# Kernel optimization log

Measured on AMD Instinct MI355X. Metric: run time of the kernel, lower is better.

Reference implementation:

```python
import jax, jax.numpy as jnp
import numpy as np
from jax.ops import segment_sum

N = 100000
E = 1600000
IN_DIM = 128
HID_DIM = 128
OUT_DIM = 64
BN_EPS = 1e-5


def setup_inputs() -> dict:
    key = jax.random.key(0)
    ks = jax.random.split(key, 8)
    h = jax.random.normal(ks[0], (N, IN_DIM), dtype=jnp.float32)
    src = jax.random.randint(ks[1], (E,), 0, N, dtype=jnp.int32)
    dst = jax.random.randint(ks[2], (E,), 0, N, dtype=jnp.int32)
    # GraphConv weights (glorot-ish scale)
    W1 = jax.random.normal(ks[3], (IN_DIM, HID_DIM), dtype=jnp.float32) / np.sqrt(IN_DIM)
    b1 = jnp.zeros((HID_DIM,), dtype=jnp.float32)
    W2 = jax.random.normal(ks[4], (HID_DIM, OUT_DIM), dtype=jnp.float32) / np.sqrt(HID_DIM)
    b2 = jnp.zeros((OUT_DIM,), dtype=jnp.float32)
    gamma = jnp.ones((HID_DIM,), dtype=jnp.float32)
    beta = jnp.zeros((HID_DIM,), dtype=jnp.float32)
    return {"h": h, "W1": W1, "b1": b1, "W2": W2, "b2": b2,
            "gamma": gamma, "beta": beta, "src": src, "dst": dst}


def _graph_conv(h, W, b, src, dst):
    # DGL GraphConv, norm='both':
    # out = D_dst^{-1/2} * A^T (D_src^{-1/2} * h) W + b, degrees clamped to >=1
    ones = jnp.ones((E,), dtype=h.dtype)
    deg_out = jnp.clip(segment_sum(ones, src, num_segments=N), 1.0)  # out-degree of src
    deg_in = jnp.clip(segment_sum(ones, dst, num_segments=N), 1.0)   # in-degree of dst
    h = h * jax.lax.rsqrt(deg_out)[:, None]
    # apply weight before aggregation when it reduces/keeps dim (DGL optimization)
    if W.shape[0] >= W.shape[1]:
        h = h @ W
        agg = segment_sum(h[src], dst, num_segments=N)  # [N, out_feat]
    else:
        agg = segment_sum(h[src], dst, num_segments=N) @ W
    return agg * jax.lax.rsqrt(deg_in)[:, None] + b


def reference(h, W1, b1, W2, b2, gamma, beta, src, dst):
    h = _graph_conv(h, W1, b1, src, dst)           # [N, HID_DIM]
    # BatchNorm1d, training mode: batch stats over node axis, biased variance
    mean = jnp.mean(h, axis=0)
    var = jnp.mean((h - mean) ** 2, axis=0)
    h = (h - mean) * jax.lax.rsqrt(var + BN_EPS) * gamma + beta
    h = jax.nn.relu(h)
    # dropout p=0.0 -> identity
    h = _graph_conv(h, W2, b2, src, dst)           # [N, OUT_DIM]
    return h
```

## Files before the change

kernel.cpp:

```cpp
#include <hip/hip_runtime.h>

#define NN 100000
#define NE 1600000
#define NB 391
#define CAP 5120
#define EPB 4096
#define NG1 6250
#define BN_EPS 1e-5f

typedef _Float16 f16;
typedef _Float16 f16x4 __attribute__((ext_vector_type(4)));
typedef _Float16 f16x8 __attribute__((ext_vector_type(8)));
typedef float f32x4v __attribute__((ext_vector_type(4)));

__global__ __launch_bounds__(256) void kInit(const float* __restrict__ W1,
                                             const float* __restrict__ W2,
                                             f16* __restrict__ W1t,
                                             f16* __restrict__ W2t,
                                             int* __restrict__ curD,
                                             int* __restrict__ curS,
                                             float* __restrict__ stats) {
    int idx = blockIdx.x * 256 + threadIdx.x;
    if (idx < NB) { curD[idx] = idx * CAP; curS[idx] = idx * CAP; }
    if (idx < 512) stats[idx] = 0.f;
    if (idx < 16384) {
        int n = idx >> 7, k = idx & 127;
        W1t[idx] = (f16)W1[k * 128 + n];
    } else if (idx < 24576) {
        int j = idx - 16384;
        int n = j >> 7, k = j & 127;
        W2t[j] = (f16)W2[k * 64 + n];
    }
}

__global__ __launch_bounds__(256) void kC(const int* __restrict__ src,
                                          const int* __restrict__ dst,
                                          int* __restrict__ curD,
                                          int* __restrict__ curS,
                                          unsigned* __restrict__ pairs,
                                          unsigned char* __restrict__ srcBuck) {
    __shared__ int sA[EPB], dA[EPB];
    __shared__ int hD[NB], hS[NB], bD_[NB], bS_[NB];
    int t = threadIdx.x;
    for (int i = t; i < NB; i += 256) { hD[i] = 0; hS[i] = 0; }
    __syncthreads();
    int e0 = blockIdx.x * EPB;
    int ne = min(EPB, NE - e0);
    for (int i = t; i < ne; i += 256) {
        int s = src[e0 + i], d = dst[e0 + i];
        sA[i] = s; dA[i] = d;
        atomicAdd(&hD[d >> 8], 1);
        atomicAdd(&hS[s >> 8], 1);
    }
    __syncthreads();
    for (int i = t; i < NB; i += 256) {
        bD_[i] = hD[i] ? atomicAdd(&curD[i], hD[i]) : 0;
        bS_[i] = hS[i] ? atomicAdd(&curS[i], hS[i]) : 0;
        hD[i] = 0; hS[i] = 0;
    }
    __syncthreads();
    for (int i = t; i < ne; i += 256) {
        int s = sA[i], d = dA[i];
        int db = d >> 8, sb = s >> 8;
        int rD = atomicAdd(&hD[db], 1);
        int posD = bD_[db] + rD;
        int limD = (db + 1) * CAP - 1;
        if (posD > limD) posD = limD;
        pairs[posD] = ((unsigned)s << 8) | (unsigned)(d & 255);
        int rS = atomicAdd(&hS[sb], 1);
        int posS = bS_[sb] + rS;
        int limS = (sb + 1) * CAP - 1;
        if (posS > limS) posS = limS;
        srcBuck[posS] = (unsigned char)(s & 255);
    }
}

__global__ __launch_bounds__(256) void kDE(const unsigned* __restrict__ pairs,
                                           const unsigned char* __restrict__ srcBuck,
                                           const int* __restrict__ curD,
                                           const int* __restrict__ curS,
                                           int* __restrict__ rowS,
                                           int* __restrict__ rowE,
                                           int* __restrict__ col,
                                           int* __restrict__ degO) {
    __shared__ unsigned bufA[CAP], bufB[CAP];
    __shared__ int binC[256], binS[256];
    __shared__ int cnt[256], csc[256];
    int t = threadIdx.x;
    if (blockIdx.x < NB) {
        int b = blockIdx.x;
        int p0 = b * CAP;
        int n = min(curD[b] - p0, CAP);
        binC[t] = 0; cnt[t] = 0;
        __syncthreads();
        for (int i = t; i < n; i += 256) {
            unsigned v = pairs[p0 + i];
            bufA[i] = v;
            atomicAdd(&binC[v >> 17], 1);
            atomicAdd(&cnt[v & 255u], 1);
        }
        __syncthreads();
        int vB = binC[t], vN = cnt[t];
        binS[t] = vB; csc[t] = vN;
        __syncthreads();
        for (int off = 1; off < 256; off <<= 1) {
            int xB = (t >= off) ? binS[t - off] : 0;
            int xN = (t >= off) ? csc[t - off] : 0;
            __syncthreads();
            binS[t] += xB; csc[t] += xN;
            __syncthreads();
        }
        int node = b * 256 + t;
        int nodeStart = csc[t] - vN;
        if (node < NN) { rowS[node] = p0 + nodeStart; rowE[node] = p0 + nodeStart + vN; }
        binC[t] = binS[t] - vB;
        cnt[t] = nodeStart;
        __syncthreads();
        for (int i = t; i < n; i += 256) {
            unsigned v = bufA[i];
            int pos = atomicAdd(&binC[v >> 17], 1);
            bufB[pos] = v;
        }
        __syncthreads();
        for (int i = t; i < n; i += 256) {
            unsigned v = bufB[i];
            int r = atomicAdd(&cnt[v & 255u], 1);
            col[p0 + r] = (int)(v >> 8);
        }
    } else {
        int b = blockIdx.x - NB;
        cnt[t] = 0;
        __syncthreads();
        int p0 = b * CAP;
        int p1 = min(curS[b], p0 + CAP);
        for (int p = p0 + t; p < p1; p += 256)
            atomicAdd(&cnt[srcBuck[p]], 1);
        __syncthreads();
        int node = b * 256 + t;
        if (node < NN) degO[node] = cnt[t];
    }
}

__global__ __launch_bounds__(256) void k_gemm1(const float* __restrict__ h,
                                               const f16* __restrict__ W1t,
                                               const int* __restrict__ degO,
                                               f16* __restrict__ x1h) {
    __shared__ f16 Ah[128 * 128];
    __shared__ f16 Bt[128 * 128];
    __shared__ float rsA[128];
    int tid = threadIdx.x;
    int row0 = blockIdx.x * 128;
    if (tid < 128) {
        int r = row0 + tid;
        float d = (r < NN) ? (float)degO[r] : 1.f;
        rsA[tid] = rsqrtf(fmaxf(d, 1.f));
    }
#pragma unroll
    for (int p = 0; p < 8; ++p) {
        int fi = p * 256 + tid;
        int r = fi >> 4, c = fi & 15;
        uint4 v = *(const uint4*)&W1t[fi * 8];
        *(uint4*)&Bt[r * 128 + ((c ^ (r & 7)) * 8)] = v;
    }
    __syncthreads();
#pragma unroll
    for (int p = 0; p < 16; ++p) {
        int fi = p * 256 + tid;
        int r = fi >> 5, c4 = fi & 31;
        int grow = row0 + r;
        float4 av = float4{0.f, 0.f, 0.f, 0.f};
        if (grow < NN) av = *(const float4*)&h[(size_t)grow * 128 + c4 * 4];
        float rs = rsA[r];
        f16x4 t;
        t[0] = (f16)(av.x * rs); t[1] = (f16)(av.y * rs);
        t[2] = (f16)(av.z * rs); t[3] = (f16)(av.w * rs);
        int c8 = c4 >> 1, off = (c4 & 1) * 4;
        *(f16x4*)&Ah[r * 128 + ((c8 ^ (r & 7)) * 8) + off] = t;
    }
    __syncthreads();
    int l = tid & 63, w = tid >> 6;
    int lr = l & 15, g = l >> 4;
    int m0 = w * 32;
    f16x8 a[2][4];
#pragma unroll
    for (int m = 0; m < 2; ++m)
#pragma unroll
        for (int kk = 0; kk < 4; ++kk) {
            int row = m0 + m * 16 + lr;
            a[m][kk] = *(f16x8*)&Ah[row * 128 + (((kk * 4 + g) ^ (row & 7)) * 8)];
        }
    f32x4v acc[2][8];
#pragma unroll
    for (int m = 0; m < 2; ++m)
#pragma unroll
        for (int n = 0; n < 8; ++n) acc[m][n] = f32x4v{0.f, 0.f, 0.f, 0.f};
#pragma unroll
    for (int n = 0; n < 8; ++n) {
        int colr = n * 16 + lr;
        f16x8 b[4];
#pragma unroll
        for (int kk = 0; kk < 4; ++kk)
            b[kk] = *(f16x8*)&Bt[colr * 128 + (((kk * 4 + g) ^ (colr & 7)) * 8)];
#pragma unroll
        for (int m = 0; m < 2; ++m)
#pragma unroll
            for (int kk = 0; kk < 4; ++kk)
                acc[m][n] = __builtin_amdgcn_mfma_f32_16x16x32_f16(a[m][kk], b[kk], acc[m][n], 0, 0, 0);
    }
    __syncthreads();
#pragma unroll
    for (int m = 0; m < 2; ++m)
#pragma unroll
        for (int n = 0; n < 8; ++n)
#pragma unroll
            for (int q = 0; q < 4; ++q) {
                int row = m0 + m * 16 + g * 4 + q;
                Ah[row * 128 + n * 16 + lr] = (f16)acc[m][n][q];
            }
    __syncthreads();
#pragma unroll
    for (int p = 0; p < 8; ++p) {
        int idx = p * 64 + l;
        int r = idx >> 4, c = idx & 15;
        int row = m0 + r, grow = row0 + row;
        uint4 v = *(uint4*)&Ah[row * 128 + c * 8];
        if (grow < NN) *(uint4*)&x1h[(size_t)grow * 128 + c * 8] = v;
    }
}

__global__ __launch_bounds__(256) void k_gather1(const f16* __restrict__ x1h,
                                                 const int* __restrict__ rowS,
                                                 const int* __restrict__ rowE,
                                                 const int* __restrict__ col,
                                                 const float* __restrict__ b1,
                                                 f16* __restrict__ y1h,
                                                 float* __restrict__ part) {
    __shared__ float red[4 * 16 * 16];
    int tid = threadIdx.x;
    int bid = blockIdx.x;
    int node = bid * 16 + (tid >> 4);
    int f8 = tid & 15;
    int s0 = rowS[node], s1 = rowE[node];
    const uint4* x4 = (const uint4*)x1h;
    float acc[8] = {0.f, 0.f, 0.f, 0.f, 0.f, 0.f, 0.f, 0.f};
    int j = s0;
    for (; j + 3 < s1; j += 4) {
        int a0 = col[j], a1 = col[j + 1], a2 = col[j + 2], a3 = col[j + 3];
        uint4 v0 = x4[(size_t)a0 * 16 + f8];
        uint4 v1 = x4[(size_t)a1 * 16 + f8];
        uint4 v2 = x4[(size_t)a2 * 16 + f8];
        uint4 v3 = x4[(size_t)a3 * 16 + f8];
        const f16* h0 = (const f16*)&v0; const f16* h1 = (const f16*)&v1;
        const f16* h2 = (const f16*)&v2; const f16* h3 = (const f16*)&v3;
#pragma unroll
        for (int k = 0; k < 8; ++k)
            acc[k] += (float)h0[k] + (float)h1[k] + (float)h2[k] + (float)h3[k];
    }
    for (; j < s1; ++j) {
        int a = col[j];
        uint4 v = x4[(size_t)a * 16 + f8];
        const f16* hp = (const f16*)&v;
#pragma unroll
        for (int k = 0; k < 8; ++k) acc[k] += (float)hp[k];
    }
    float rs = rsqrtf(fmaxf((float)(s1 - s0), 1.f));
    const float4* b4 = (const float4*)b1;
    float4 ba = b4[f8 * 2], bb = b4[f8 * 2 + 1];
    f16x8 o;
    o[0] = (f16)(acc[0] * rs + ba.x); o[1] = (f16)(acc[1] * rs + ba.y);
    o[2] = (f16)(acc[2] * rs + ba.z); o[3] = (f16)(acc[3] * rs + ba.w);
    o[4] = (f16)(acc[4] * rs + bb.x); o[5] = (f16)(acc[5] * rs + bb.y);
    o[6] = (f16)(acc[6] * rs + bb.z); o[7] = (f16)(acc[7] * rs + bb.w);
    *(f16x8*)&y1h[(size_t)node * 128 + f8 * 8] = o;
    float sv[8], qv[8];
#pragma unroll
    for (int k = 0; k < 8; ++k) { sv[k] = (float)o[k]; qv[k] = sv[k] * sv[k]; }
#pragma unroll
    for (int mask = 16; mask <= 32; mask <<= 1) {
#pragma unroll
        for (int k = 0; k < 8; ++k) {
            sv[k] += __shfl_xor(sv[k], mask);
            qv[k] += __shfl_xor(qv[k], mask);
        }
    }
    int w = tid >> 6, lane = tid & 63;
    if (lane < 16) {
#pragma unroll
        for (int k = 0; k < 8; ++k) {
            red[w * 256 + lane * 16 + k] = sv[k];
            red[w * 256 + lane * 16 + 8 + k] = qv[k];
        }
    }
    __syncthreads();
    int f8_ = tid & 15, idx = tid >> 4;
    float tot = red[0 * 256 + f8_ * 16 + idx] + red[1 * 256 + f8_ * 16 + idx]
              + red[2 * 256 + f8_ * 16 + idx] + red[3 * 256 + f8_ * 16 + idx];
    int slot = (idx < 8) ? (f8_ * 8 + idx) : (128 + f8_ * 8 + (idx - 8));
    part[(size_t)bid * 256 + slot] = tot;
}

__global__ __launch_bounds__(256) void k_bnred(const float* __restrict__ part,
                                               float* __restrict__ stats) {
    int t = threadIdx.x;
    float loc = 0.f;
    for (int b = blockIdx.x; b < NG1; b += gridDim.x)
        loc += part[(size_t)b * 256 + t];
    atomicAdd(&stats[t], loc);
}

__global__ __launch_bounds__(128) void k_bnfinal(float* __restrict__ stats,
                                                 const float* __restrict__ gamma,
                                                 const float* __restrict__ beta) {
    int f = threadIdx.x;
    float mean = stats[f] * (1.f / NN);
    float var = stats[128 + f] * (1.f / NN) - mean * mean;
    var = fmaxf(var, 0.f);
    float sc = gamma[f] * rsqrtf(var + BN_EPS);
    stats[256 + f] = sc;
    stats[384 + f] = beta[f] - mean * sc;
}

__global__ __launch_bounds__(256) void k_gemm2(const f16* __restrict__ y1h,
                                               const f16* __restrict__ W2t,
                                               const int* __restrict__ degO,
                                               const float* __restrict__ stats,
                                               f16* __restrict__ x2h) {
    __shared__ f16 Ah[128 * 128];
    __shared__ f16 Bt[64 * 128];
    __shared__ float sc[128], sh[128], rsA[128];
    int tid = threadIdx.x;
    int row0 = blockIdx.x * 128;
    if (tid < 128) {
        sc[tid] = stats[256 + tid];
        sh[tid] = stats[384 + tid];
        int r = row0 + tid;
        float d = (r < NN) ? (float)degO[r] : 1.f;
        rsA[tid] = rsqrtf(fmaxf(d, 1.f));
    }
#pragma unroll
    for (int p = 0; p < 4; ++p) {
        int fi = p * 256 + tid;
        int r = fi >> 4, c = fi & 15;
        uint4 v = *(const uint4*)&W2t[fi * 8];
        *(uint4*)&Bt[r * 128 + ((c ^ (r & 7)) * 8)] = v;
    }
    __syncthreads();
#pragma unroll
    for (int p = 0; p < 8; ++p) {
        int fi = p * 256 + tid;
        int r = fi >> 4, c = fi & 15;
        int grow = row0 + r;
        f16x8 t;
        if (grow < NN) {
            uint4 v = *(const uint4*)&y1h[(size_t)grow * 128 + c * 8];
            const f16* hp = (const f16*)&v;
            float rs = rsA[r];
#pragma unroll
            for (int i = 0; i < 8; ++i) {
                int ch = c * 8 + i;
                float x = (float)hp[i] * sc[ch] + sh[ch];
                t[i] = (f16)(fmaxf(x, 0.f) * rs);
            }
        } else {
#pragma unroll
            for (int i = 0; i < 8; ++i) t[i] = (f16)0.f;
        }
        *(f16x8*)&Ah[r * 128 + ((c ^ (r & 7)) * 8)] = t;
    }
    __syncthreads();
    int l = tid & 63, w = tid >> 6;
    int lr = l & 15, g = l >> 4;
    int m0 = w * 32;
    f16x8 a[2][4];
#pragma unroll
    for (int m = 0; m < 2; ++m)
#pragma unroll
        for (int kk = 0; kk < 4; ++kk) {
            int row = m0 + m * 16 + lr;
            a[m][kk] = *(f16x8*)&Ah[row * 128 + (((kk * 4 + g) ^ (row & 7)) * 8)];
        }
    f32x4v acc[2][4];
#pragma unroll
    for (int m = 0; m < 2; ++m)
#pragma unroll
        for (int n = 0; n < 4; ++n) acc[m][n] = f32x4v{0.f, 0.f, 0.f, 0.f};
#pragma unroll
    for (int n = 0; n < 4; ++n) {
        int colr = n * 16 + lr;
        f16x8 b[4];
#pragma unroll
        for (int kk = 0; kk < 4; ++kk)
            b[kk] = *(f16x8*)&Bt[colr * 128 + (((kk * 4 + g) ^ (colr & 7)) * 8)];
#pragma unroll
        for (int m = 0; m < 2; ++m)
#pragma unroll
            for (int kk = 0; kk < 4; ++kk)
                acc[m][n] = __builtin_amdgcn_mfma_f32_16x16x32_f16(a[m][kk], b[kk], acc[m][n], 0, 0, 0);
    }
    __syncthreads();
#pragma unroll
    for (int m = 0; m < 2; ++m)
#pragma unroll
        for (int n = 0; n < 4; ++n)
#pragma unroll
            for (int q = 0; q < 4; ++q) {
                int row = m0 + m * 16 + g * 4 + q;
                Ah[row * 64 + n * 16 + lr] = (f16)acc[m][n][q];
            }
    __syncthreads();
#pragma unroll
    for (int p = 0; p < 4; ++p) {
        int idx = p * 64 + l;
        int r = idx >> 3, c = idx & 7;
        int row = m0 + r, grow = row0 + row;
        uint4 v = *(uint4*)&Ah[row * 64 + c * 8];
        if (grow < NN) *(uint4*)&x2h[(size_t)grow * 64 + c * 8] = v;
    }
}

__global__ __launch_bounds__(256) void k_gather2(const f16* __restrict__ x2h,
                                                 const int* __restrict__ rowS,
                                                 const int* __restrict__ rowE,
                                                 const int* __restrict__ col,
                                                 const float* __restrict__ b2,
                                                 float* __restrict__ out) {
    int node = blockIdx.x * 32 + (threadIdx.x >> 3);
    int f8 = threadIdx.x & 7;
    if (node >= NN) return;
    int s0 = rowS[node], s1 = rowE[node];
    const uint4* x4 = (const uint4*)x2h;
    float acc[8] = {0.f, 0.f, 0.f, 0.f, 0.f, 0.f, 0.f, 0.f};
    int j = s0;
    for (; j + 3 < s1; j += 4) {
        uint4 v[4];
#pragma unroll
        for (int u = 0; u < 4; ++u)
            v[u] = x4[(size_t)col[j + u] * 8 + f8];
#pragma unroll
        for (int u = 0; u < 4; ++u) {
            const f16* hp = (const f16*)&v[u];
#pragma unroll
            for (int k = 0; k < 8; ++k) acc[k] += (float)hp[k];
        }
    }
    for (; j < s1; ++j) {
        uint4 v = x4[(size_t)col[j] * 8 + f8];
        const f16* hp = (const f16*)&v;
#pragma unroll
        for (int k = 0; k < 8; ++k) acc[k] += (float)hp[k];
    }
    float rs = rsqrtf(fmaxf((float)(s1 - s0), 1.f));
    const float4* b4 = (const float4*)b2;
    float4 ba = b4[f8 * 2], bb = b4[f8 * 2 + 1];
    float4 o0, o1;
    o0.x = acc[0] * rs + ba.x; o0.y = acc[1] * rs + ba.y;
    o0.z = acc[2] * rs + ba.z; o0.w = acc[3] * rs + ba.w;
    o1.x = acc[4] * rs + bb.x; o1.y = acc[5] * rs + bb.y;
    o1.z = acc[6] * rs + bb.z; o1.w = acc[7] * rs + bb.w;
    *(float4*)&out[(size_t)node * 64 + f8 * 8] = o0;
    *(float4*)&out[(size_t)node * 64 + f8 * 8 + 4] = o1;
}

extern "C" void kernel_launch(void* const* d_in, const int* in_sizes, int n_in,
                              void* d_out, int out_size, void* d_ws, size_t ws_size,
                              hipStream_t stream) {
    const float* h     = (const float*)d_in[0];
    const float* W1    = (const float*)d_in[1];
    const float* b1    = (const float*)d_in[2];
    const float* W2    = (const float*)d_in[3];
    const float* b2    = (const float*)d_in[4];
    const float* gamma = (const float*)d_in[5];
    const float* beta  = (const float*)d_in[6];
    const int*   src   = (const int*)d_in[7];
    const int*   dst   = (const int*)d_in[8];
    float* out = (float*)d_out;

    const size_t BSZ = (size_t)NB * CAP;

    int* base = (int*)d_ws;
    float* stats = (float*)base;
    int* curD = base + 512;
    int* curS = curD + NB;
    int* rowS = curS + NB;
    int* rowE = rowS + NN;
    int* degO = rowE + NN;
    int* col  = degO + NN;
    unsigned* pairs = (unsigned*)(col + BSZ);
    unsigned char* srcBuck = (unsigned char*)(pairs + BSZ);
    float* part = (float*)(pairs + BSZ + (BSZ + 3) / 4);
    size_t o = (size_t)(col + BSZ - base) + BSZ + (BSZ + 3) / 4 + (size_t)NG1 * 256;
    o = (o + 3) & ~(size_t)3;
    f16* W1t = (f16*)(base + o);
    f16* W2t = W1t + 16384;
    o += 8192 + 4096;
    f16* x1h = (f16*)(base + o);
    o += (size_t)NN * 64;
    f16* y1h = (f16*)(base + o);
    f16* x2h = x1h;

    kInit<<<97, 256, 0, stream>>>(W1, W2, W1t, W2t, curD, curS, stats);

    int bgrid = (NE + EPB - 1) / EPB;
    kC<<<bgrid, 256, 0, stream>>>(src, dst, curD, curS, pairs, srcBuck);
    kDE<<<2 * NB, 256, 0, stream>>>(pairs, srcBuck, curD, curS, rowS, rowE, col, degO);

    int ggrid = (NN + 127) / 128;
    k_gemm1<<<ggrid, 256, 0, stream>>>(h, W1t, degO, x1h);
    k_gather1<<<NG1, 256, 0, stream>>>(x1h, rowS, rowE, col, b1, y1h, part);
    k_bnred<<<64, 256, 0, stream>>>(part, stats);
    k_bnfinal<<<1, 128, 0, stream>>>(stats, gamma, beta);
    k_gemm2<<<ggrid, 256, 0, stream>>>(y1h, W2t, degO, stats, x2h);
    k_gather2<<<(NN + 31) / 32, 256, 0, stream>>>(x2h, rowS, rowE, col, b2, out);
}
```

Baseline: 253.3 us.

## Fuse BN reduce and finalize, drop source-bin presort, enlarge edge bucketing blocks

After: 252.6 us. No clear change (-0.3%).

```diff
diff --git a/kernel.cpp b/kernel.cpp
--- a/kernel.cpp
+++ b/kernel.cpp
@@ -4,8 +4,9 @@
 #define NE 1600000
 #define NB 391
 #define CAP 5120
-#define EPB 4096
+#define EPB 8192
 #define NG1 6250
+#define NBN 64
 #define BN_EPS 1e-5f
 
 typedef _Float16 f16;
@@ -19,10 +20,12 @@
                                              f16* __restrict__ W2t,
                                              int* __restrict__ curD,
                                              int* __restrict__ curS,
-                                             float* __restrict__ stats) {
+                                             float* __restrict__ stats,
+                                             int* __restrict__ done) {
     int idx = blockIdx.x * 256 + threadIdx.x;
     if (idx < NB) { curD[idx] = idx * CAP; curS[idx] = idx * CAP; }
     if (idx < 512) stats[idx] = 0.f;
+    if (idx == 512) done[0] = 0;
     if (idx < 16384) {
         int n = idx >> 7, k = idx & 127;
         W1t[idx] = (f16)W1[k * 128 + n];
@@ -33,7 +36,7 @@
     }
 }
 
-__global__ __launch_bounds__(256) void kC(const int* __restrict__ src,
+__global__ __launch_bounds__(512) void kC(const int* __restrict__ src,
                                           const int* __restrict__ dst,
                                           int* __restrict__ curD,
                                           int* __restrict__ curS,
@@ -42,24 +45,24 @@
     __shared__ int sA[EPB], dA[EPB];
     __shared__ int hD[NB], hS[NB], bD_[NB], bS_[NB];
     int t = threadIdx.x;
-    for (int i = t; i < NB; i += 256) { hD[i] = 0; hS[i] = 0; }
+    for (int i = t; i < NB; i += 512) { hD[i] = 0; hS[i] = 0; }
     __syncthreads();
     int e0 = blockIdx.x * EPB;
     int ne = min(EPB, NE - e0);
-    for (int i = t; i < ne; i += 256) {
+    for (int i = t; i < ne; i += 512) {
         int s = src[e0 + i], d = dst[e0 + i];
         sA[i] = s; dA[i] = d;
         atomicAdd(&hD[d >> 8], 1);
         atomicAdd(&hS[s >> 8], 1);
     }
     __syncthreads();
-    for (int i = t; i < NB; i += 256) {
+    for (int i = t; i < NB; i += 512) {
         bD_[i] = hD[i] ? atomicAdd(&curD[i], hD[i]) : 0;
         bS_[i] = hS[i] ? atomicAdd(&curS[i], hS[i]) : 0;
         hD[i] = 0; hS[i] = 0;
     }
     __syncthreads();
-    for (int i = t; i < ne; i += 256) {
+    for (int i = t; i < ne; i += 512) {
         int s = sA[i], d = dA[i];
         int db = d >> 8, sb = s >> 8;
         int rD = atomicAdd(&hD[db], 1);
@@ -83,47 +86,37 @@
                                            int* __restrict__ rowE,
                                            int* __restrict__ col,
                                            int* __restrict__ degO) {
-    __shared__ unsigned bufA[CAP], bufB[CAP];
-    __shared__ int binC[256], binS[256];
+    __shared__ unsigned bufA[CAP];
     __shared__ int cnt[256], csc[256];
     int t = threadIdx.x;
     if (blockIdx.x < NB) {
         int b = blockIdx.x;
         int p0 = b * CAP;
         int n = min(curD[b] - p0, CAP);
-        binC[t] = 0; cnt[t] = 0;
+        cnt[t] = 0;
         __syncthreads();
         for (int i = t; i < n; i += 256) {
             unsigned v = pairs[p0 + i];
             bufA[i] = v;
-            atomicAdd(&binC[v >> 17], 1);
             atomicAdd(&cnt[v & 255u], 1);
         }
         __syncthreads();
-        int vB = binC[t], vN = cnt[t];
-        binS[t] = vB; csc[t] = vN;
+        int vN = cnt[t];
+        csc[t] = vN;
         __syncthreads();
         for (int off = 1; off < 256; off <<= 1) {
-            int xB = (t >= off) ? binS[t - off] : 0;
-            int xN = (t >= off) ? csc[t - off] : 0;
+            int x = (t >= off) ? csc[t - off] : 0;
             __syncthreads();
-            binS[t] += xB; csc[t] += xN;
+            csc[t] += x;
             __syncthreads();
         }
+        int nodeStart = csc[t] - vN;
         int node = b * 256 + t;
-        int nodeStart = csc[t] - vN;
         if (node < NN) { rowS[node] = p0 + nodeStart; rowE[node] = p0 + nodeStart + vN; }
-        binC[t] = binS[t] - vB;
         cnt[t] = nodeStart;
         __syncthreads();
         for (int i = t; i < n; i += 256) {
             unsigned v = bufA[i];
-            int pos = atomicAdd(&binC[v >> 17], 1);
-            bufB[pos] = v;
-        }
-        __syncthreads();
-        for (int i = t; i < n; i += 256) {
-            unsigned v = bufB[i];
             int r = atomicAdd(&cnt[v & 255u], 1);
             col[p0 + r] = (int)(v >> 8);
         }
@@ -299,25 +292,30 @@
     part[(size_t)bid * 256 + slot] = tot;
 }
 
-__global__ __launch_bounds__(256) void k_bnred(const float* __restrict__ part,
-                                               float* __restrict__ stats) {
+__global__ __launch_bounds__(256) void k_bnfin(const float* __restrict__ part,
+                                               float* __restrict__ stats,
+                                               int* __restrict__ done,
+                                               const float* __restrict__ gamma,
+                                               const float* __restrict__ beta) {
     int t = threadIdx.x;
     float loc = 0.f;
     for (int b = blockIdx.x; b < NG1; b += gridDim.x)
         loc += part[(size_t)b * 256 + t];
     atomicAdd(&stats[t], loc);
-}
-
-__global__ __launch_bounds__(128) void k_bnfinal(float* __restrict__ stats,
-                                                 const float* __restrict__ gamma,
-                                                 const float* __restrict__ beta) {
-    int f = threadIdx.x;
-    float mean = stats[f] * (1.f / NN);
-    float var = stats[128 + f] * (1.f / NN) - mean * mean;
-    var = fmaxf(var, 0.f);
-    float sc = gamma[f] * rsqrtf(var + BN_EPS);
-    stats[256 + f] = sc;
-    stats[384 + f] = beta[f] - mean * sc;
+    __threadfence();
+    __shared__ int amLast;
+    if (t == 0) amLast = (atomicAdd(done, 1) == NBN - 1) ? 1 : 0;
+    __syncthreads();
+    if (amLast && t < 128) {
+        float s  = __hip_atomic_load(&stats[t], __ATOMIC_RELAXED, __HIP_MEMORY_SCOPE_AGENT);
+        float sq = __hip_atomic_load(&stats[128 + t], __ATOMIC_RELAXED, __HIP_MEMORY_SCOPE_AGENT);
+        float mean = s * (1.f / NN);
+        float var = sq * (1.f / NN) - mean * mean;
+        var = fmaxf(var, 0.f);
+        float sc = gamma[t] * rsqrtf(var + BN_EPS);
+        stats[256 + t] = sc;
+        stats[384 + t] = beta[t] - mean * sc;
+    }
 }
 
 __global__ __launch_bounds__(256) void k_gemm2(const f16* __restrict__ y1h,
@@ -479,7 +477,8 @@
 
     int* base = (int*)d_ws;
     float* stats = (float*)base;
-    int* curD = base + 512;
+    int* done = base + 512;
+    int* curD = base + 513;
     int* curS = curD + NB;
     int* rowS = curS + NB;
     int* rowE = rowS + NN;
@@ -498,17 +497,16 @@
     f16* y1h = (f16*)(base + o);
     f16* x2h = x1h;
 
-    kInit<<<97, 256, 0, stream>>>(W1, W2, W1t, W2t, curD, curS, stats);
+    kInit<<<97, 256, 0, stream>>>(W1, W2, W1t, W2t, curD, curS, stats, done);
 
     int bgrid = (NE + EPB - 1) / EPB;
-    kC<<<bgrid, 256, 0, stream>>>(src, dst, curD, curS, pairs, srcBuck);
+    kC<<<bgrid, 512, 0, stream>>>(src, dst, curD, curS, pairs, srcBuck);
     kDE<<<2 * NB, 256, 0, stream>>>(pairs, srcBuck, curD, curS, rowS, rowE, col, degO);
 
     int ggrid = (NN + 127) / 128;
     k_gemm1<<<ggrid, 256, 0, stream>>>(h, W1t, degO, x1h);
     k_gather1<<<NG1, 256, 0, stream>>>(x1h, rowS, rowE, col, b1, y1h, part);
-    k_bnred<<<64, 256, 0, stream>>>(part, stats);
-    k_bnfinal<<<1, 128, 0, stream>>>(stats, gamma, beta);
+    k_bnfin<<<NBN, 256, 0, stream>>>(part, stats, done, gamma, beta);
     k_gemm2<<<ggrid, 256, 0, stream>>>(y1h, W2t, degO, stats, x2h);
     k_gather2<<<(NN + 31) / 32, 256, 0, stream>>>(x2h, rowS, rowE, col, b2, out);
 }
```
